# Optimization experiments

Hardware: AMD Instinct MI355X
Metric: run time of the kernel (lower is better)

Reference implementation:

```python
import jax, jax.numpy as jnp
import numpy as np

NEG_RATIO = 3.0
IOU_THR = 0.5
ALPHA = 1.0


def _cxcywh_to_xyxy(b):
    return jnp.concatenate([b[..., :2] - b[..., 2:] / 2, b[..., :2] + b[..., 2:] / 2], -1)


def _box_iou(a, b):  # a: [G,4] xyxy, b: [A,4] xyxy -> [G,A]
    lt = jnp.maximum(a[:, None, :2], b[None, :, :2])
    rb = jnp.minimum(a[:, None, 2:], b[None, :, 2:])
    wh = jnp.clip(rb - lt, 0.0)
    inter = wh[..., 0] * wh[..., 1]
    area_a = (a[:, 2] - a[:, 0]) * (a[:, 3] - a[:, 1])
    area_b = (b[:, 2] - b[:, 0]) * (b[:, 3] - b[:, 1])
    return inter / (area_a[:, None] + area_b[None, :] - inter)


def _encode(gt, anc):  # both cxcywh, last dim 4
    g_cxcy = (gt[..., :2] - anc[..., :2]) / anc[..., 2:]
    g_wh = jnp.log(gt[..., 2:]) - jnp.log(anc[..., 2:])
    return jnp.concatenate([g_cxcy, g_wh], -1)


def _match_one(boxes, labels, anchors):
    # boxes: [G,4] cxcywh, labels: [G] int, anchors: [A,4] cxcywh -> [A,5]
    ious = _box_iou(_cxcywh_to_xyxy(boxes), _cxcywh_to_xyxy(anchors))  # [G,A]
    best_gt_ov = ious.max(0)
    best_gt_idx = ious.argmax(0)  # [A]
    over = best_gt_ov > IOU_THR  # [A]
    lab_f = labels.astype(anchors.dtype)
    # anchors over threshold take their best gt, encoded w.r.t. that anchor
    enc_per_anchor = _encode(boxes[best_gt_idx], anchors)  # [A,4]
    ph = jnp.where(over[:, None],
                   jnp.concatenate([enc_per_anchor, lab_f[best_gt_idx][:, None]], -1),
                   0.0)  # [A,5]
    # every gt also claims its best anchor
    best_prior_idx = ious.argmax(1)  # [G]
    enc_best = _encode(boxes, anchors[best_prior_idx])  # [G,4]
    y2 = jnp.concatenate([enc_best, lab_f[:, None]], -1)
    return ph.at[best_prior_idx].set(y2)


def _multibox_loss(loc_pred, conf_pred, anchors, gt_boxes, gt_labels):
    B, A, C = conf_pred.shape
    target = jax.vmap(_match_one, in_axes=(0, 0, None))(gt_boxes, gt_labels, anchors)  # [B,A,5]
    pos = (target[:, :, 4:5] > 0).astype(loc_pred.dtype)  # [B,A,1]
    num_pos = pos.sum(axis=1, keepdims=True)  # [B,1,1]
    N = pos.sum()
    # smooth L1 on masked locations (beta=1), sum reduction
    d = pos * loc_pred - pos * target[:, :, :4]
    ad = jnp.abs(d)
    loc_loss = jnp.where(ad < 1.0, 0.5 * d * d, ad - 0.5).sum()
    # hard negative mining
    num_neg = jnp.minimum(NEG_RATIO * num_pos, A - 1)  # [B,1,1]
    lse = jax.scipy.special.logsumexp(conf_pred, axis=-1, keepdims=True)  # [B,A,1]
    idx01 = (target[:, :, 4:5] != 0).astype(jnp.int32)  # faithful: gathers class 0 or 1
    gathered = jnp.take_along_axis(conf_pred, idx01, axis=-1)  # [B,A,1]
    cls_l = (lse - gathered) * (1.0 - pos)  # zero-out positives
    order = jnp.argsort(-cls_l, axis=1)  # descending sort indices
    rank = jnp.argsort(order, axis=1)  # rank of each box's loss
    neg_mask = rank < num_neg
    sampled = jnp.logical_or(pos > 0, neg_mask)  # [B,A,1]
    s = sampled.astype(conf_pred.dtype)
    logits = (s * conf_pred).reshape(-1, C)
    labels_ce = (s * target[:, :, 4:5]).reshape(-1).astype(jnp.int32)
    lse2 = jax.scipy.special.logsumexp(logits, axis=-1)
    picked = jnp.take_along_axis(logits, labels_ce[:, None], axis=1)[:, 0]
    cls_loss = (lse2 - picked).sum()
    return (loc_loss + ALPHA * cls_loss) / N


def setup_inputs() -> dict:
    key = jax.random.key(0)
    k1, k2, k3, k4, k5, k6, k7 = jax.random.split(key, 7)
    B, A, C, G = 64, 8732, 81, 32
    loc_pred = jax.random.normal(k1, (B, A, 4), jnp.float32)
    conf_pred = jax.random.normal(k2, (B, A, C), jnp.float32)
    anc_cxcy = jax.random.uniform(k3, (A, 2), jnp.float32)
    anc_wh = jax.random.uniform(k4, (A, 2), jnp.float32) * 0.48 + 0.02
    anchors = jnp.concatenate([anc_cxcy, anc_wh], -1)
    gt_cxcy = jax.random.uniform(k5, (B, G, 2), jnp.float32) * 0.8 + 0.1
    gt_wh = jax.random.uniform(k6, (B, G, 2), jnp.float32) * 0.35 + 0.05
    gt_boxes = jnp.concatenate([gt_cxcy, gt_wh], -1)
    gt_labels = jax.random.randint(k7, (B, G), 0, C - 1, jnp.int32) + 1  # labels in 1..C-1
    return {"loc_pred": loc_pred, "conf_pred": conf_pred, "anchors": anchors,
            "gt_boxes": gt_boxes, "gt_labels": gt_labels}


def reference(loc_pred, conf_pred, anchors, gt_boxes, gt_labels):
    return _multibox_loss(loc_pred, conf_pred, anchors, gt_boxes, gt_labels)
```

## Files before the change

### kernel.cpp

```cpp
#include <hip/hip_runtime.h>
#include <math.h>

#pragma clang fp contract(off)

#define BB 64
#define AA 8732
#define CC 81
#define GG 32
#define A_BLOCKS 35
#define KA1_BLOCKS (BB*A_BLOCKS)
#define KA2_BLOCKS (BB*GG/4)
#define ROWS_PC 64
#define KC_BLOCKS (BB*AA/ROWS_PC)
#define CHUNK_F4 (ROWS_PC*81/4)


__global__ __launch_bounds__(256) void kAC(const float* __restrict__ anchors,
    const float* __restrict__ gt_boxes, const float* __restrict__ conf,
    unsigned char* __restrict__ bestg, unsigned int* __restrict__ bestp,
    float* __restrict__ cls_l, unsigned int* __restrict__ ticket,
    double* __restrict__ btot_acc, int* __restrict__ np_acc)
{
    __shared__ float buf[ROWS_PC * 81];
    int tid = threadIdx.x;
    if (blockIdx.x == 0 && tid == 0) {
        *ticket = 0u; *btot_acc = 0.0; *np_acc = 0;
    }
    if (blockIdx.x < KA1_BLOCKS) {
        int blk = blockIdx.x;
        int b = blk / A_BLOCKS, ca = blk % A_BLOCKS;
        int a = ca * 256 + tid;
        float4* gco = (float4*)buf;
        float* gar = buf + GG * 4;
        if (tid < GG) {
            float4 gb = ((const float4*)gt_boxes)[b * GG + tid];
            float x1 = gb.x - gb.z / 2.0f, y1 = gb.y - gb.w / 2.0f;
            float x2 = gb.x + gb.z / 2.0f, y2 = gb.y + gb.w / 2.0f;
            gco[tid] = make_float4(x1, y1, x2, y2);
            gar[tid] = (x2 - x1) * (y2 - y1);
        }
        __syncthreads();
        if (a >= AA) return;
        float4 an = ((const float4*)anchors)[a];
        float ax1 = an.x - an.z / 2.0f, ay1 = an.y - an.w / 2.0f;
        float ax2 = an.x + an.z / 2.0f, ay2 = an.y + an.w / 2.0f;
        float aar = (ax2 - ax1) * (ay2 - ay1);
        float bi = -1.0f, bu = 1.0f; int bgi = 0;
#pragma unroll
        for (int g = 0; g < GG; ++g) {
            float4 c = gco[g];
            float ltx = fmaxf(c.x, ax1), lty = fmaxf(c.y, ay1);
            float rbx = fminf(c.z, ax2), rby = fminf(c.w, ay2);
            float w = fmaxf(rbx - ltx, 0.0f), h = fmaxf(rby - lty, 0.0f);
            float inter = w * h;
            float uni = gar[g] + aar - inter;
            if (inter * bu > bi * uni) { bi = inter; bu = uni; bgi = g; }
        }
        bestg[b * AA + a] = (2.0f * bi > bu) ? (unsigned char)bgi : (unsigned char)0xFF;
    } else if (blockIdx.x < KA1_BLOCKS + KA2_BLOCKS) {
        int wv = tid >> 6, lane = tid & 63;
        int pair = (blockIdx.x - KA1_BLOCKS) * 4 + wv;
        int b = pair >> 5, g = pair & 31;
        float4 gb = ((const float4*)gt_boxes)[b * GG + g];
        float gx1 = gb.x - gb.z / 2.0f, gy1 = gb.y - gb.w / 2.0f;
        float gx2 = gb.x + gb.z / 2.0f, gy2 = gb.y + gb.w / 2.0f;
        float gar2 = (gx2 - gx1) * (gy2 - gy1);
        float bi = -1.0f, bu = 1.0f; int ba = 0;
        for (int a = lane; a < AA; a += 64) {
            float4 an = ((const float4*)anchors)[a];
            float ax1 = an.x - an.z / 2.0f, ay1 = an.y - an.w / 2.0f;
            float ax2 = an.x + an.z / 2.0f, ay2 = an.y + an.w / 2.0f;
            float aar = (ax2 - ax1) * (ay2 - ay1);
            float ltx = fmaxf(gx1, ax1), lty = fmaxf(gy1, ay1);
            float rbx = fminf(gx2, ax2), rby = fminf(gy2, ay2);
            float w = fmaxf(rbx - ltx, 0.0f), h = fmaxf(rby - lty, 0.0f);
            float inter = w * h;
            float uni = gar2 + aar - inter;
            if (inter * bu > bi * uni) { bi = inter; bu = uni; ba = a; }
        }
#pragma unroll
        for (int off = 32; off > 0; off >>= 1) {
            float oi = __shfl_down(bi, off);
            float ou = __shfl_down(bu, off);
            int   oa = __shfl_down(ba, off);
            float p1 = oi * bu, p2 = bi * ou;
            bool take = (p1 > p2) || ((p1 == p2) && (oa < ba));
            if (take) { bi = oi; bu = ou; ba = oa; }
        }
        if (lane == 0) bestp[pair] = (unsigned int)ba;
    } else {
        int chunk = blockIdx.x - KA1_BLOCKS - KA2_BLOCKS;
        const float4* __restrict__ src4 = (const float4*)conf;
        size_t base4 = (size_t)chunk * CHUNK_F4;
        float4* buf4 = (float4*)buf;
#pragma unroll
        for (int i = 0; i < 5; ++i) buf4[tid + 256 * i] = src4[base4 + tid + 256 * i];
        if (tid < CHUNK_F4 - 1280) buf4[1280 + tid] = src4[base4 + 1280 + tid];
        __syncthreads();
        int r = tid >> 2, q = tid & 3;
        const float* row = buf + r * 81;
        int kstart = (q == 0) ? 0 : 21 + (q - 1) * 20;
        float s = 0.0f;
#pragma unroll
        for (int k = 0; k < 20; ++k) s += __expf(row[kstart + k]);
        if (q == 0) s += __expf(row[20]);
        s += __shfl_xor(s, 1);
        s += __shfl_xor(s, 2);
        if (q == 0)
            cls_l[chunk * ROWS_PC + r] = __logf(s) - row[0];
    }
}

__global__ __launch_bounds__(1024) void kBDE(const float* __restrict__ anchors,
    const float* __restrict__ gt_boxes, const int* __restrict__ gt_labels,
    const float* __restrict__ loc_pred, const unsigned char* __restrict__ bestg,
    const unsigned int* __restrict__ bestp, const float* __restrict__ cls_l,
    const float* __restrict__ conf, unsigned int* __restrict__ ticket,
    double* __restrict__ btot_acc, int* __restrict__ np_acc,
    float* __restrict__ out)
{
    int b = blockIdx.x, tid = threadIdx.x;
    __shared__ int forced[AA];
    __shared__ unsigned char slab[AA];
    __shared__ unsigned int whist[16 * 256];
    __shared__ unsigned int hist[256];
    __shared__ float gcx[GG], gcy[GG], gw[GG], gh[GG];
    __shared__ int glab[GG];
    __shared__ double red_d[16];
    __shared__ int red_i[16];
    __shared__ unsigned int red_u[16];
    __shared__ unsigned int sh_prefix, sh_remaining;
    __shared__ int sh_np;
    __shared__ double sh_loc;
    unsigned int* cl = (unsigned int*)forced;

    for (int i = tid; i < AA; i += 1024) forced[i] = -1;
    if (tid < GG) {
        float4 gb = ((const float4*)gt_boxes)[b * GG + tid];
        gcx[tid] = gb.x; gcy[tid] = gb.y; gw[tid] = gb.z; gh[tid] = gb.w;
        glab[tid] = gt_labels[b * GG + tid];
    }
    __syncthreads();
    if (tid < GG)
        atomicMax(&forced[(int)bestp[b * GG + tid]], tid);
    __syncthreads();

    double lsum = 0.0; int pcount = 0;
    for (int a = tid; a < AA; a += 1024) {
        int gf = forced[a];
        int gsel;
        if (gf >= 0) gsel = gf;
        else {
            unsigned char bg = bestg[b * AA + a];
            gsel = (bg == 0xFF) ? -1 : (int)bg;
        }
        int lab = 0;
        if (gsel >= 0) {
            lab = glab[gsel];
            float4 an = ((const float4*)anchors)[a];
            float e0 = (gcx[gsel] - an.x) / an.z;
            float e1 = (gcy[gsel] - an.y) / an.w;
            float e2 = logf(gw[gsel]) - logf(an.z);
            float e3 = logf(gh[gsel]) - logf(an.w);
            float4 lp = ((const float4*)loc_pred)[b * AA + a];
            float d0 = lp.x - e0, d1 = lp.y - e1, d2 = lp.z - e2, d3 = lp.w - e3;
            float t = 0.0f, ad;
            ad = fabsf(d0); t += (ad < 1.0f) ? 0.5f * d0 * d0 : ad - 0.5f;
            ad = fabsf(d1); t += (ad < 1.0f) ? 0.5f * d1 * d1 : ad - 0.5f;
            ad = fabsf(d2); t += (ad < 1.0f) ? 0.5f * d2 * d2 : ad - 0.5f;
            ad = fabsf(d3); t += (ad < 1.0f) ? 0.5f * d3 * d3 : ad - 0.5f;
            lsum += (double)t;
            pcount++;
        }
        slab[a] = (unsigned char)lab;
    }
#pragma unroll
    for (int off = 32; off > 0; off >>= 1) {
        lsum += __shfl_down(lsum, off);
        pcount += __shfl_down(pcount, off);
    }
    if ((tid & 63) == 0) { red_d[tid >> 6] = lsum; red_i[tid >> 6] = pcount; }
    __syncthreads();
    if (tid == 0) {
        double L = 0.0; int P = 0;
        for (int w = 0; w < 16; ++w) { L += red_d[w]; P += red_i[w]; }
        sh_loc = L; sh_np = P;
    }
    __syncthreads();
    int np_ = sh_np;

    double pc = 0.0;
    const float* src = cls_l + b * AA;
    for (int i = tid; i < AA; i += 1024) {
        int lab = slab[i];
        float sv = src[i];
        if (lab > 0) {
            size_t rowb = ((size_t)(b * AA + i)) * 81;
            pc += (double)(sv + conf[rowb] - conf[rowb + lab]);
            cl[i] = 0u;
        } else {
            cl[i] = __float_as_uint(fmaxf(sv, 0.0f));
        }
    }
#pragma unroll
    for (int off = 32; off > 0; off >>= 1) pc += __shfl_down(pc, off);
    if ((tid & 63) == 0) red_d[tid >> 6] = pc;
    __syncthreads();
    double sum_pos = 0.0;
    int k = min(3 * np_, AA - 1);
    if (tid == 0) {
        for (int w = 0; w < 16; ++w) sum_pos += red_d[w];
        sh_prefix = 0u; sh_remaining = (unsigned int)k;
    }
    __syncthreads();

    double topk = 0.0;
    int p_t_pos = 0;
    if (k > 0) {
        for (int shift = 24; shift >= 0; shift -= 8) {
            for (int j = tid; j < 4096; j += 1024) whist[j] = 0u;
            __syncthreads();
            unsigned int mask = (shift == 24) ? 0u : (0xFFFFFFFFu << (shift + 8));
            unsigned int pre = sh_prefix;
            unsigned int* myh = whist + (tid >> 6) * 256;
            for (int i = tid; i < AA; i += 1024) {
                unsigned int u = cl[i];
                if ((u & mask) == pre) atomicAdd(&myh[(u >> shift) & 255], 1u);
            }
            __syncthreads();
            if (tid < 256) {
                unsigned int t = 0;
#pragma unroll
                for (int w = 0; w < 16; ++w) t += whist[w * 256 + tid];
                hist[tid] = t;
            }
            __syncthreads();
            if (tid < 64) {
                int l = tid;
                unsigned int h4 = hist[4 * l] + hist[4 * l + 1]
                                + hist[4 * l + 2] + hist[4 * l + 3];
                unsigned int S = h4;
#pragma unroll
                for (int off = 1; off < 64; off <<= 1) {
                    unsigned int o = __shfl_down(S, off);
                    S += (l + off < 64) ? o : 0u;
                }
                unsigned int rem = sh_remaining;
                unsigned long long ball = __ballot(S >= rem);
                int L = 63 - __clzll(ball);
                if (l == L) {
                    unsigned int rem2 = rem - (S - h4);
                    unsigned int c = 0;
                    for (int dd = 4 * L + 3; dd >= 4 * L; --dd) {
                        c += hist[dd];
                        if (c >= rem2) {
                            sh_prefix = pre | ((unsigned int)dd << shift);
                            sh_remaining = rem2 - (c - hist[dd]);
                            break;
                        }
                    }
                }
            }
            __syncthreads();
        }
        unsigned int vbits = sh_prefix;
        unsigned int myc = 0; double mys = 0.0;
        for (int i = tid; i < AA; i += 1024) {
            unsigned int u = cl[i];
            if (u > vbits) { myc++; mys += (double)__uint_as_float(u); }
        }
#pragma unroll
        for (int off = 32; off > 0; off >>= 1) {
            myc += __shfl_down(myc, off);
            mys += __shfl_down(mys, off);
        }
        if ((tid & 63) == 0) { red_u[tid >> 6] = myc; red_d[tid >> 6] = mys; }
        __syncthreads();
        if (tid == 0) {
            unsigned int cnt_gt = 0; double sum_gt = 0.0;
            for (int w = 0; w < 16; ++w) { cnt_gt += red_u[w]; sum_gt += red_d[w]; }
            topk = sum_gt + (double)(k - (int)cnt_gt) * (double)__uint_as_float(vbits);
            if (vbits == 0u) {
                int t = k - (int)cnt_gt, c2 = 0;
                for (int i = 0; i < AA && c2 < t; ++i) {
                    if (cl[i] == 0u) { c2++; if (slab[i] > 0) p_t_pos++; }
                }
            }
        }
    }
    if (tid == 0) {
        int unsampled = AA - np_ - k + p_t_pos;
        double clsb = sum_pos + topk + (double)unsampled * (double)logf(81.0f);
        double myb = sh_loc + clsb;
        atomicAdd(btot_acc, myb);
        atomicAdd(np_acc, np_);
        __threadfence();
        unsigned int t = atomicAdd(ticket, 1u);
        if (t == BB - 1) {
            double tt = atomicAdd(btot_acc, 0.0);
            int nn = atomicAdd(np_acc, 0);
            out[0] = (float)(tt / (double)nn);
        }
    }
}

extern "C" void kernel_launch(void* const* d_in, const int* in_sizes, int n_in,
                              void* d_out, int out_size, void* d_ws, size_t ws_size,
                              hipStream_t stream) {
    (void)in_sizes; (void)n_in; (void)out_size; (void)ws_size;
    const float* loc_pred  = (const float*)d_in[0];
    const float* conf_pred = (const float*)d_in[1];
    const float* anchors   = (const float*)d_in[2];
    const float* gt_boxes  = (const float*)d_in[3];
    const int*   gt_labels = (const int*)d_in[4];

    char* ws = (char*)d_ws;
    unsigned int*  bestp    = (unsigned int*)(ws + 0);
    unsigned char* bestg    = (unsigned char*)(ws + 8192);
    float*         cls_l    = (float*)(ws + 567040);
    unsigned int*  ticket   = (unsigned int*)(ws + 2802432);
    double*        btot_acc = (double*)(ws + 2802440);
    int*           np_acc   = (int*)(ws + 2802448);

    kAC <<<KA1_BLOCKS + KA2_BLOCKS + KC_BLOCKS, 256, 0, stream>>>(
        anchors, gt_boxes, conf_pred, bestg, bestp, cls_l, ticket, btot_acc, np_acc);
    kBDE<<<BB, 1024, 0, stream>>>(anchors, gt_boxes, gt_labels, loc_pred,
        bestg, bestp, cls_l, conf_pred, ticket, btot_acc, np_acc, (float*)d_out);
}
```

Before: 323.4 us.

## Split fused kernels into four stages to parallelize per-batch matching and mining

The combined matching+logsumexp kernel is split into a matching kernel and a persistent, double-buffered logsumexp kernel over the conf tensor. The per-batch 1024-thread matching/loss pass now runs as 8 segments per batch across 512 blocks. Each block writes mining keys and labels to global memory and accumulates per-batch sums with atomics, and a separate top-k kernel reloads them. The aim is to lift the occupancy limit of 64 large blocks doing serial work, at the cost of extra launches, global round-trips for keys and labels, and a 32-way bestp scan per anchor.

Result: no change. 323.2 us (-0.1%).

```diff
diff --git a/kernel.cpp b/kernel.cpp
--- a/kernel.cpp
+++ b/kernel.cpp
@@ -10,28 +10,49 @@
 #define A_BLOCKS 35
 #define KA1_BLOCKS (BB*A_BLOCKS)
 #define KA2_BLOCKS (BB*GG/4)
+#define KA_BLOCKS (KA1_BLOCKS+KA2_BLOCKS)
 #define ROWS_PC 64
-#define KC_BLOCKS (BB*AA/ROWS_PC)
+#define KC_CHUNKS (BB*AA/ROWS_PC)
 #define CHUNK_F4 (ROWS_PC*81/4)
-
-
-__global__ __launch_bounds__(256) void kAC(const float* __restrict__ anchors,
-    const float* __restrict__ gt_boxes, const float* __restrict__ conf,
-    unsigned char* __restrict__ bestg, unsigned int* __restrict__ bestp,
-    float* __restrict__ cls_l, unsigned int* __restrict__ ticket,
-    double* __restrict__ btot_acc, int* __restrict__ np_acc)
-{
-    __shared__ float buf[ROWS_PC * 81];
+#define KC_GRID 768
+#define KB_SEGS 8
+#define KB_BLOCKS (BB*KB_SEGS)
+#define SEGSZ 1092
+
+
+__device__ __forceinline__ void iou_upd(const float4 an, int a,
+    float gx1, float gy1, float gx2, float gy2, float gar2,
+    float& bi, float& bu, int& ba)
+{
+    float ax1 = an.x - an.z / 2.0f, ay1 = an.y - an.w / 2.0f;
+    float ax2 = an.x + an.z / 2.0f, ay2 = an.y + an.w / 2.0f;
+    float aar = (ax2 - ax1) * (ay2 - ay1);
+    float ltx = fmaxf(gx1, ax1), lty = fmaxf(gy1, ay1);
+    float rbx = fminf(gx2, ax2), rby = fminf(gy2, ay2);
+    float w = fmaxf(rbx - ltx, 0.0f), h = fmaxf(rby - lty, 0.0f);
+    float inter = w * h;
+    float uni = gar2 + aar - inter;
+    if (inter * bu > bi * uni) { bi = inter; bu = uni; ba = a; }
+}
+
+__global__ __launch_bounds__(256) void kA(const float* __restrict__ anchors,
+    const float* __restrict__ gt_boxes, unsigned char* __restrict__ bestg,
+    unsigned int* __restrict__ bestp, int* __restrict__ num_pos,
+    double* __restrict__ loc_sum, double* __restrict__ cls_pos,
+    unsigned int* __restrict__ ticket, double* __restrict__ btot_acc,
+    int* __restrict__ np_acc)
+{
     int tid = threadIdx.x;
-    if (blockIdx.x == 0 && tid == 0) {
-        *ticket = 0u; *btot_acc = 0.0; *np_acc = 0;
+    if (blockIdx.x == 0) {
+        if (tid < BB) { num_pos[tid] = 0; loc_sum[tid] = 0.0; cls_pos[tid] = 0.0; }
+        if (tid == 0) { *ticket = 0u; *btot_acc = 0.0; *np_acc = 0; }
     }
     if (blockIdx.x < KA1_BLOCKS) {
+        __shared__ float4 gco[GG];
+        __shared__ float gar[GG];
         int blk = blockIdx.x;
         int b = blk / A_BLOCKS, ca = blk % A_BLOCKS;
         int a = ca * 256 + tid;
-        float4* gco = (float4*)buf;
-        float* gar = buf + GG * 4;
         if (tid < GG) {
             float4 gb = ((const float4*)gt_boxes)[b * GG + tid];
             float x1 = gb.x - gb.z / 2.0f, y1 = gb.y - gb.w / 2.0f;
@@ -57,7 +78,7 @@
             if (inter * bu > bi * uni) { bi = inter; bu = uni; bgi = g; }
         }
         bestg[b * AA + a] = (2.0f * bi > bu) ? (unsigned char)bgi : (unsigned char)0xFF;
-    } else if (blockIdx.x < KA1_BLOCKS + KA2_BLOCKS) {
+    } else {
         int wv = tid >> 6, lane = tid & 63;
         int pair = (blockIdx.x - KA1_BLOCKS) * 4 + wv;
         int b = pair >> 5, g = pair & 31;
@@ -65,18 +86,22 @@
         float gx1 = gb.x - gb.z / 2.0f, gy1 = gb.y - gb.w / 2.0f;
         float gx2 = gb.x + gb.z / 2.0f, gy2 = gb.y + gb.w / 2.0f;
         float gar2 = (gx2 - gx1) * (gy2 - gy1);
+        const float4* __restrict__ A4 = (const float4*)anchors;
         float bi = -1.0f, bu = 1.0f; int ba = 0;
-        for (int a = lane; a < AA; a += 64) {
-            float4 an = ((const float4*)anchors)[a];
-            float ax1 = an.x - an.z / 2.0f, ay1 = an.y - an.w / 2.0f;
-            float ax2 = an.x + an.z / 2.0f, ay2 = an.y + an.w / 2.0f;
-            float aar = (ax2 - ax1) * (ay2 - ay1);
-            float ltx = fmaxf(gx1, ax1), lty = fmaxf(gy1, ay1);
-            float rbx = fminf(gx2, ax2), rby = fminf(gy2, ay2);
-            float w = fmaxf(rbx - ltx, 0.0f), h = fmaxf(rby - lty, 0.0f);
-            float inter = w * h;
-            float uni = gar2 + aar - inter;
-            if (inter * bu > bi * uni) { bi = inter; bu = uni; ba = a; }
+        for (int k0 = 0; k0 < 136; k0 += 4) {
+            int a0 = lane + 64 * k0;
+            float4 v0 = A4[a0];
+            float4 v1 = A4[a0 + 64];
+            float4 v2 = A4[a0 + 128];
+            float4 v3 = A4[a0 + 192];
+            iou_upd(v0, a0,       gx1, gy1, gx2, gy2, gar2, bi, bu, ba);
+            iou_upd(v1, a0 + 64,  gx1, gy1, gx2, gy2, gar2, bi, bu, ba);
+            iou_upd(v2, a0 + 128, gx1, gy1, gx2, gy2, gar2, bi, bu, ba);
+            iou_upd(v3, a0 + 192, gx1, gy1, gx2, gy2, gar2, bi, bu, ba);
+        }
+        if (lane < 28) {
+            int a = 8704 + lane;
+            iou_upd(A4[a], a, gx1, gy1, gx2, gy2, gar2, bi, bu, ba);
         }
 #pragma unroll
         for (int off = 32; off > 0; off >>= 1) {
@@ -88,66 +113,94 @@
             if (take) { bi = oi; bu = ou; ba = oa; }
         }
         if (lane == 0) bestp[pair] = (unsigned int)ba;
-    } else {
-        int chunk = blockIdx.x - KA1_BLOCKS - KA2_BLOCKS;
-        const float4* __restrict__ src4 = (const float4*)conf;
-        size_t base4 = (size_t)chunk * CHUNK_F4;
-        float4* buf4 = (float4*)buf;
-#pragma unroll
-        for (int i = 0; i < 5; ++i) buf4[tid + 256 * i] = src4[base4 + tid + 256 * i];
-        if (tid < CHUNK_F4 - 1280) buf4[1280 + tid] = src4[base4 + 1280 + tid];
+    }
+}
+
+__global__ __launch_bounds__(256) void kC(const float* __restrict__ conf,
+    float* __restrict__ cls_l)
+{
+    __shared__ float buf[2][ROWS_PC * 81];
+    int tid = threadIdx.x;
+    const float4* __restrict__ src4 = (const float4*)conf;
+    float4 r0, r1, r2, r3, r4, r5;
+    int chunk = blockIdx.x;
+    {
+        size_t b4i = (size_t)chunk * CHUNK_F4;
+        r0 = src4[b4i + tid];        r1 = src4[b4i + tid + 256];
+        r2 = src4[b4i + tid + 512];  r3 = src4[b4i + tid + 768];
+        r4 = src4[b4i + tid + 1024];
+        if (tid < 16) r5 = src4[b4i + tid + 1280];
+        float4* w4 = (float4*)buf[0];
+        w4[tid] = r0; w4[tid + 256] = r1; w4[tid + 512] = r2;
+        w4[tid + 768] = r3; w4[tid + 1024] = r4;
+        if (tid < 16) w4[tid + 1280] = r5;
+    }
+    int cur = 0;
+    for (;;) {
+        int next = chunk + KC_GRID;
+        bool hn = next < KC_CHUNKS;
         __syncthreads();
-        int r = tid >> 2, q = tid & 3;
-        const float* row = buf + r * 81;
-        int kstart = (q == 0) ? 0 : 21 + (q - 1) * 20;
-        float s = 0.0f;
-#pragma unroll
-        for (int k = 0; k < 20; ++k) s += __expf(row[kstart + k]);
-        if (q == 0) s += __expf(row[20]);
-        s += __shfl_xor(s, 1);
-        s += __shfl_xor(s, 2);
-        if (q == 0)
-            cls_l[chunk * ROWS_PC + r] = __logf(s) - row[0];
-    }
-}
-
-__global__ __launch_bounds__(1024) void kBDE(const float* __restrict__ anchors,
+        if (hn) {
+            size_t b4i = (size_t)next * CHUNK_F4;
+            r0 = src4[b4i + tid];        r1 = src4[b4i + tid + 256];
+            r2 = src4[b4i + tid + 512];  r3 = src4[b4i + tid + 768];
+            r4 = src4[b4i + tid + 1024];
+            if (tid < 16) r5 = src4[b4i + tid + 1280];
+        }
+        {
+            int r = tid >> 2, q = tid & 3;
+            const float* row = buf[cur] + r * 81;
+            int kstart = (q == 0) ? 0 : 21 + (q - 1) * 20;
+            float s = 0.0f;
+#pragma unroll
+            for (int k = 0; k < 20; ++k) s += __expf(row[kstart + k]);
+            if (q == 0) s += __expf(row[20]);
+            s += __shfl_xor(s, 1);
+            s += __shfl_xor(s, 2);
+            if (q == 0)
+                cls_l[chunk * ROWS_PC + r] = __logf(s) - row[0];
+        }
+        if (!hn) break;
+        {
+            float4* w4 = (float4*)buf[cur ^ 1];
+            w4[tid] = r0; w4[tid + 256] = r1; w4[tid + 512] = r2;
+            w4[tid + 768] = r3; w4[tid + 1024] = r4;
+            if (tid < 16) w4[tid + 1280] = r5;
+        }
+        chunk = next; cur ^= 1;
+    }
+}
+
+__global__ __launch_bounds__(256) void kB(const float* __restrict__ anchors,
     const float* __restrict__ gt_boxes, const int* __restrict__ gt_labels,
     const float* __restrict__ loc_pred, const unsigned char* __restrict__ bestg,
     const unsigned int* __restrict__ bestp, const float* __restrict__ cls_l,
-    const float* __restrict__ conf, unsigned int* __restrict__ ticket,
-    double* __restrict__ btot_acc, int* __restrict__ np_acc,
-    float* __restrict__ out)
-{
-    int b = blockIdx.x, tid = threadIdx.x;
-    __shared__ int forced[AA];
-    __shared__ unsigned char slab[AA];
-    __shared__ unsigned int whist[16 * 256];
-    __shared__ unsigned int hist[256];
+    const float* __restrict__ conf, unsigned int* __restrict__ keyg,
+    unsigned char* __restrict__ labg, int* __restrict__ num_pos,
+    double* __restrict__ loc_sum, double* __restrict__ cls_pos)
+{
+    int tid = threadIdx.x;
+    int b = blockIdx.x >> 3, seg = blockIdx.x & 7;
     __shared__ float gcx[GG], gcy[GG], gw[GG], gh[GG];
     __shared__ int glab[GG];
-    __shared__ double red_d[16];
-    __shared__ int red_i[16];
-    __shared__ unsigned int red_u[16];
-    __shared__ unsigned int sh_prefix, sh_remaining;
-    __shared__ int sh_np;
-    __shared__ double sh_loc;
-    unsigned int* cl = (unsigned int*)forced;
-
-    for (int i = tid; i < AA; i += 1024) forced[i] = -1;
+    __shared__ unsigned int bp[GG];
+    __shared__ double rd[4], rp[4];
+    __shared__ int ri[4];
     if (tid < GG) {
         float4 gb = ((const float4*)gt_boxes)[b * GG + tid];
         gcx[tid] = gb.x; gcy[tid] = gb.y; gw[tid] = gb.z; gh[tid] = gb.w;
         glab[tid] = gt_labels[b * GG + tid];
+        bp[tid] = bestp[b * GG + tid];
     }
     __syncthreads();
-    if (tid < GG)
-        atomicMax(&forced[(int)bestp[b * GG + tid]], tid);
-    __syncthreads();
-
-    double lsum = 0.0; int pcount = 0;
-    for (int a = tid; a < AA; a += 1024) {
-        int gf = forced[a];
+
+    int aend = (seg + 1) * SEGSZ; if (aend > AA) aend = AA;
+    double lsum = 0.0, pc = 0.0; int pcount = 0;
+    for (int a = seg * SEGSZ + tid; a < aend; a += 256) {
+        int gf = -1;
+#pragma unroll
+        for (int g = 0; g < GG; ++g)
+            if (bp[g] == (unsigned int)a) gf = g;
         int gsel;
         if (gf >= 0) gsel = gf;
         else {
@@ -172,46 +225,54 @@
             lsum += (double)t;
             pcount++;
         }
-        slab[a] = (unsigned char)lab;
+        labg[b * AA + a] = (unsigned char)lab;
+        float sv = cls_l[b * AA + a];
+        unsigned int key;
+        if (lab > 0) {
+            size_t rowb = ((size_t)(b * AA + a)) * 81;
+            pc += (double)(sv + conf[rowb] - conf[rowb + lab]);
+            key = 0u;
+        } else {
+            key = __float_as_uint(fmaxf(sv, 0.0f));
+        }
+        keyg[b * AA + a] = key;
     }
 #pragma unroll
     for (int off = 32; off > 0; off >>= 1) {
         lsum += __shfl_down(lsum, off);
+        pc += __shfl_down(pc, off);
         pcount += __shfl_down(pcount, off);
     }
-    if ((tid & 63) == 0) { red_d[tid >> 6] = lsum; red_i[tid >> 6] = pcount; }
+    if ((tid & 63) == 0) { rd[tid >> 6] = lsum; rp[tid >> 6] = pc; ri[tid >> 6] = pcount; }
     __syncthreads();
     if (tid == 0) {
-        double L = 0.0; int P = 0;
-        for (int w = 0; w < 16; ++w) { L += red_d[w]; P += red_i[w]; }
-        sh_loc = L; sh_np = P;
-    }
-    __syncthreads();
-    int np_ = sh_np;
-
-    double pc = 0.0;
-    const float* src = cls_l + b * AA;
-    for (int i = tid; i < AA; i += 1024) {
-        int lab = slab[i];
-        float sv = src[i];
-        if (lab > 0) {
-            size_t rowb = ((size_t)(b * AA + i)) * 81;
-            pc += (double)(sv + conf[rowb] - conf[rowb + lab]);
-            cl[i] = 0u;
-        } else {
-            cl[i] = __float_as_uint(fmaxf(sv, 0.0f));
-        }
-    }
-#pragma unroll
-    for (int off = 32; off > 0; off >>= 1) pc += __shfl_down(pc, off);
-    if ((tid & 63) == 0) red_d[tid >> 6] = pc;
-    __syncthreads();
-    double sum_pos = 0.0;
+        double L = rd[0] + rd[1] + rd[2] + rd[3];
+        double C = rp[0] + rp[1] + rp[2] + rp[3];
+        int P = ri[0] + ri[1] + ri[2] + ri[3];
+        if (P) atomicAdd(&num_pos[b], P);
+        atomicAdd(&loc_sum[b], L);
+        atomicAdd(&cls_pos[b], C);
+    }
+}
+
+__global__ __launch_bounds__(1024, 4) void kE(const unsigned int* __restrict__ keyg,
+    const unsigned char* __restrict__ labg, const int* __restrict__ num_pos,
+    const double* __restrict__ loc_sum, const double* __restrict__ cls_pos,
+    unsigned int* __restrict__ ticket, double* __restrict__ btot_acc,
+    int* __restrict__ np_acc, float* __restrict__ out)
+{
+    int b = blockIdx.x, tid = threadIdx.x;
+    __shared__ unsigned int cl[AA];
+    __shared__ unsigned int whist[16 * 256];
+    __shared__ unsigned int hist[256];
+    __shared__ double red_d[16];
+    __shared__ unsigned int red_u[16];
+    __shared__ unsigned int sh_prefix, sh_remaining;
+
+    for (int i = tid; i < AA; i += 1024) cl[i] = keyg[b * AA + i];
+    int np_ = num_pos[b];
     int k = min(3 * np_, AA - 1);
-    if (tid == 0) {
-        for (int w = 0; w < 16; ++w) sum_pos += red_d[w];
-        sh_prefix = 0u; sh_remaining = (unsigned int)k;
-    }
+    if (tid == 0) { sh_prefix = 0u; sh_remaining = (unsigned int)k; }
     __syncthreads();
 
     double topk = 0.0;
@@ -283,15 +344,15 @@
             if (vbits == 0u) {
                 int t = k - (int)cnt_gt, c2 = 0;
                 for (int i = 0; i < AA && c2 < t; ++i) {
-                    if (cl[i] == 0u) { c2++; if (slab[i] > 0) p_t_pos++; }
+                    if (cl[i] == 0u) { c2++; if (labg[b * AA + i] > 0) p_t_pos++; }
                 }
             }
         }
     }
     if (tid == 0) {
         int unsampled = AA - np_ - k + p_t_pos;
-        double clsb = sum_pos + topk + (double)unsampled * (double)logf(81.0f);
-        double myb = sh_loc + clsb;
+        double clsb = cls_pos[b] + topk + (double)unsampled * (double)logf(81.0f);
+        double myb = loc_sum[b] + clsb;
         atomicAdd(btot_acc, myb);
         atomicAdd(np_acc, np_);
         __threadfence();
@@ -318,12 +379,20 @@
     unsigned int*  bestp    = (unsigned int*)(ws + 0);
     unsigned char* bestg    = (unsigned char*)(ws + 8192);
     float*         cls_l    = (float*)(ws + 567040);
-    unsigned int*  ticket   = (unsigned int*)(ws + 2802432);
-    double*        btot_acc = (double*)(ws + 2802440);
-    int*           np_acc   = (int*)(ws + 2802448);
-
-    kAC <<<KA1_BLOCKS + KA2_BLOCKS + KC_BLOCKS, 256, 0, stream>>>(
-        anchors, gt_boxes, conf_pred, bestg, bestp, cls_l, ticket, btot_acc, np_acc);
-    kBDE<<<BB, 1024, 0, stream>>>(anchors, gt_boxes, gt_labels, loc_pred,
-        bestg, bestp, cls_l, conf_pred, ticket, btot_acc, np_acc, (float*)d_out);
-}
+    unsigned int*  keyg     = (unsigned int*)(ws + 2802432);
+    unsigned char* labg     = (unsigned char*)(ws + 5037824);
+    int*           num_pos  = (int*)(ws + 5596672);
+    double*        loc_sum  = (double*)(ws + 5596928);
+    double*        cls_pos  = (double*)(ws + 5597440);
+    unsigned int*  ticket   = (unsigned int*)(ws + 5597952);
+    double*        btot_acc = (double*)(ws + 5597960);
+    int*           np_acc   = (int*)(ws + 5597968);
+
+    kA<<<KA_BLOCKS, 256, 0, stream>>>(anchors, gt_boxes, bestg, bestp,
+        num_pos, loc_sum, cls_pos, ticket, btot_acc, np_acc);
+    kC<<<KC_GRID, 256, 0, stream>>>(conf_pred, cls_l);
+    kB<<<KB_BLOCKS, 256, 0, stream>>>(anchors, gt_boxes, gt_labels, loc_pred,
+        bestg, bestp, cls_l, conf_pred, keyg, labg, num_pos, loc_sum, cls_pos);
+    kE<<<BB, 1024, 0, stream>>>(keyg, labg, num_pos, loc_sum, cls_pos,
+        ticket, btot_acc, np_acc, (float*)d_out);
+}
```
